# Performance work log

Measured on AMD Instinct MI355X. Metric: run time of the kernel, lower is better.

Reference implementation:

```python
import jax, jax.numpy as jnp
import numpy as np

N_NODES = 100000
N_EDGES = 1000000
VOCAB = 128
EMB = 64
HID = 64
N_CLASSES = 2
N_GRAPHS = 2048


def setup_inputs() -> dict:
    key = jax.random.key(0)
    ks = jax.random.split(key, 12)
    x = jax.random.randint(ks[0], (N_NODES,), 0, VOCAB)
    edge_index = jax.random.randint(ks[1], (2, N_EDGES), 0, N_NODES)
    batch = jnp.sort(jax.random.randint(ks[2], (N_NODES,), 0, N_GRAPHS))

    def glorot(k, shape):
        fan = shape[0]
        return jax.random.normal(k, shape, dtype=jnp.float32) / np.sqrt(fan).astype(np.float32)

    emb = jax.random.normal(ks[3], (VOCAB, EMB), dtype=jnp.float32)
    W1_l = glorot(ks[4], (EMB, HID)); b1 = jnp.zeros((HID,), jnp.float32)
    W1_r = glorot(ks[5], (EMB, HID))
    W2_l = glorot(ks[6], (HID, HID)); b2 = jnp.zeros((HID,), jnp.float32)
    W2_r = glorot(ks[7], (HID, HID))
    W_out = glorot(ks[8], (HID, N_CLASSES)); b_out = jnp.zeros((N_CLASSES,), jnp.float32)
    return {"x": x, "edge_index": edge_index, "batch": batch, "emb": emb,
            "W1_l": W1_l, "b1": b1, "W1_r": W1_r,
            "W2_l": W2_l, "b2": b2, "W2_r": W2_r,
            "W_out": W_out, "b_out": b_out}


def _sage_conv(h, src, dst, Wl, bl, Wr):
    # PyG SAGEConv: out = lin_l(mean_{j in N(i)} h_j) + lin_r(h_i); lin_r has no bias
    msgs = h[src]                                                        # [E, D] gather
    agg = jax.ops.segment_sum(msgs, dst, num_segments=N_NODES)          # [N, D] scatter-add
    cnt = jax.ops.segment_sum(jnp.ones((src.shape[0], 1), h.dtype), dst,
                              num_segments=N_NODES)                      # [N, 1] degree
    mean = agg / jnp.maximum(cnt, 1.0)
    return mean @ Wl + bl + h @ Wr


def reference(x, edge_index, batch, emb, W1_l, b1, W1_r, W2_l, b2, W2_r, W_out, b_out):
    src, dst = edge_index[0], edge_index[1]
    h = emb[x]                                                           # [N, EMB]
    h = jax.nn.relu(_sage_conv(h, src, dst, W1_l, b1, W1_r))             # [N, HID]
    h = jax.nn.relu(_sage_conv(h, src, dst, W2_l, b2, W2_r))             # [N, HID]
    # global_mean_pool over graph ids
    gsum = jax.ops.segment_sum(h, batch, num_segments=N_GRAPHS)          # [G, HID]
    gcnt = jax.ops.segment_sum(jnp.ones((N_NODES, 1), h.dtype), batch,
                               num_segments=N_GRAPHS)
    pooled = gsum / jnp.maximum(gcnt, 1.0)
    return pooled @ W_out + b_out                                        # [G, C]
```

## Files before the change

### kernel.cpp

```cpp
#include <hip/hip_runtime.h>
#include <hip/hip_bf16.h>

#define N_NODES 100000
#define N_EDGES 1000000
#define EMB 64
#define HID 64
#define VOCAB 128
#define N_GRAPHS 2048

#define CBUCKET 256
#define NBK ((N_NODES + CBUCKET - 1) / CBUCKET)
#define CAP 4096
#define CHUNK 4096
#define SCAT_BLOCKS ((N_EDGES + CHUNK - 1) / CHUNK)
#define GB ((N_NODES + 255) / 256)

#define BCASTF(v, l) __int_as_float(__builtin_amdgcn_readlane(__float_as_int(v), (l)))

typedef __attribute__((ext_vector_type(8))) short short8;
typedef __attribute__((ext_vector_type(4))) float f32x4;

__device__ __forceinline__ float bf2f(unsigned short u) {
    return __uint_as_float((unsigned)u << 16);
}
__device__ __forceinline__ unsigned short f2bf(float f) {
    return __bfloat16_as_ushort(__float2bfloat16(f));
}

__global__ __launch_bounds__(256) void setup_kernel(
    const int* __restrict__ batch, int* __restrict__ gstart,
    const float* __restrict__ emb, const float* __restrict__ W1l,
    const float* __restrict__ W1r,
    const float* __restrict__ W2l, const float* __restrict__ W2r,
    float* __restrict__ embW1l, float* __restrict__ embW1r,
    unsigned short* __restrict__ w2frag,
    int* __restrict__ cursor, float* __restrict__ gsum)
{
    int b = blockIdx.x;
    int t = threadIdx.x;
    if (b < GB) {
        int i = b * 256 + t;
        if (i >= N_NODES) return;
        int bg = batch[i];
        int bp = (i == 0) ? -1 : batch[i - 1];
        for (int g = bp + 1; g <= bg; ++g) gstart[g] = i;
        if (i == N_NODES - 1)
            for (int g = bg + 1; g <= N_GRAPHS; ++g) gstart[g] = N_NODES;
    } else if (b < GB + 32) {
        int vb = b - GB;
        int wave = t >> 6, lane = t & 63;
        int v = vb * 4 + wave;
        if (v < VOCAB) {
            float er = emb[v * 64 + lane];
            float al = 0.f, ar = 0.f;
#pragma unroll 8
            for (int d = 0; d < 64; ++d) {
                float e = BCASTF(er, d);
                al += e * W1l[d * 64 + lane];
                ar += e * W1r[d * 64 + lane];
            }
            embW1l[v * 64 + lane] = al;
            embW1r[v * 64 + lane] = ar;
        }
        int g = vb * 256 + t;
        int j = g & 7, l = (g >> 3) & 63, h = (g >> 9) & 1, tt = g >> 10;
        int k = h * 32 + ((l >> 4) * 8) + j;
        int n = tt * 16 + (l & 15);
        float w = (n < 64) ? W2l[k * 64 + n] : W2r[k * 64 + (n - 64)];
        w2frag[g] = f2bf(w);
    } else {
        for (int i = t; i < NBK; i += 256) cursor[i] = i * CAP;
        for (int i = t; i < N_GRAPHS * 2; i += 256) gsum[i] = 0.f;
    }
}

__global__ __launch_bounds__(256) void scatter_kernel(
    const int* __restrict__ src, const int* __restrict__ dst,
    const int* __restrict__ x,
    int* __restrict__ cursor, unsigned* __restrict__ edge8)
{
    __shared__ unsigned earr[CHUNK];
    __shared__ unsigned short karr[CHUNK];
    __shared__ int bcnt[NBK];
    __shared__ int bbase[NBK];
    int t = threadIdx.x;
    for (int i = t; i < NBK; i += 256) bcnt[i] = 0;
    __syncthreads();
    int e0 = blockIdx.x * CHUNK;
    int n = min(e0 + CHUNK, N_EDGES) - e0;
    for (int i = t; i < n; i += 256) {
        int d = dst[e0 + i];
        int s = src[e0 + i];
        int xv = x[s];
        int k = d >> 8;
        earr[i] = (unsigned)s | ((unsigned)xv << 17) | ((unsigned)(d & 255) << 24);
        karr[i] = (unsigned short)k;
        atomicAdd(&bcnt[k], 1);
    }
    __syncthreads();
    for (int i = t; i < NBK; i += 256) {
        int c = bcnt[i];
        bbase[i] = c ? atomicAdd(&cursor[i], c) : 0;
        bcnt[i] = 0;
    }
    __syncthreads();
    for (int i = t; i < n; i += 256) {
        int k = karr[i];
        int off = atomicAdd(&bcnt[k], 1);
        edge8[bbase[k] + off] = earr[i];
    }
}

__global__ __launch_bounds__(256) void csr_kernel(
    const unsigned* __restrict__ edge8, const int* __restrict__ cursor,
    int* __restrict__ row_start, int* __restrict__ deg, int* __restrict__ col)
{
    __shared__ int cnt[CBUCKET];
    __shared__ int scn[CBUCKET];
    int b = blockIdx.x;
    int t = threadIdx.x;
    int lo = b * CAP, hi = cursor[b];
    cnt[t] = 0;
    __syncthreads();
    for (int i = lo + t; i < hi; i += 256)
        atomicAdd(&cnt[edge8[i] >> 24], 1);
    __syncthreads();
    int v = cnt[t];
    scn[t] = v;
    __syncthreads();
    for (int off = 1; off < 256; off <<= 1) {
        int tmp = (t >= off) ? scn[t - off] : 0;
        __syncthreads();
        scn[t] += tmp;
        __syncthreads();
    }
    int excl = scn[t] - v;
    int node = b * CBUCKET + t;
    if (node < N_NODES) { row_start[node] = lo + excl; deg[node] = v; }
    cnt[t] = excl;
    __syncthreads();
    for (int i = lo + t; i < hi; i += 256) {
        unsigned e = edge8[i];
        int slot = atomicAdd(&cnt[e >> 24], 1);
        col[lo + slot] = (int)(e & 0xFFFFFF);
    }
}

#define S1_NPW 8
__global__ __launch_bounds__(256) void sage1_kernel(
    const int* __restrict__ x, const float* __restrict__ embW1l,
    const float* __restrict__ embW1r, const float* __restrict__ b1,
    const int* __restrict__ row_start, const int* __restrict__ deg,
    const int* __restrict__ col, unsigned short* __restrict__ h1b)
{
    __shared__ float elds[VOCAB * 64];
    int t = threadIdx.x;
    for (int i = t * 4; i < VOCAB * 64; i += 1024)
        *(float4*)&elds[i] = *(const float4*)&embW1l[i];
    __syncthreads();

    int wave = t >> 6, lane = t & 63;
    int base_node = (blockIdx.x * 4 + wave) * S1_NPW;
    float bias = b1[lane];

    int rs[S1_NPW], dgs[S1_NPW], cidx[S1_NPW], xn[S1_NPW];
    float self[S1_NPW];
#pragma unroll
    for (int n = 0; n < S1_NPW; ++n) {
        rs[n] = row_start[base_node + n];
        dgs[n] = deg[base_node + n];
        xn[n] = x[base_node + n];
    }
#pragma unroll
    for (int n = 0; n < S1_NPW; ++n) {
        cidx[n] = (lane < dgs[n]) ? col[rs[n] + lane] : 0;
        self[n] = embW1r[xn[n] * 64 + lane];
    }

    for (int n = 0; n < S1_NPW; ++n) {
        int node = base_node + n;
        int dg = dgs[n];
        int dgc = (dg < 64) ? dg : 64;

        float s0 = 0.f, s1 = 0.f, s2 = 0.f, s3 = 0.f;
        int j = 0;
        for (; j + 4 <= dgc; j += 4) {
            int x0 = __builtin_amdgcn_readlane(cidx[n], j + 0) >> 17;
            int x1 = __builtin_amdgcn_readlane(cidx[n], j + 1) >> 17;
            int x2 = __builtin_amdgcn_readlane(cidx[n], j + 2) >> 17;
            int x3 = __builtin_amdgcn_readlane(cidx[n], j + 3) >> 17;
            s0 += elds[x0 * 64 + lane];
            s1 += elds[x1 * 64 + lane];
            s2 += elds[x2 * 64 + lane];
            s3 += elds[x3 * 64 + lane];
        }
        for (; j < dgc; ++j) {
            int x0 = __builtin_amdgcn_readlane(cidx[n], j) >> 17;
            s0 += elds[x0 * 64 + lane];
        }
        for (int k = 64; k < dg; ++k) {
            int c = col[rs[n] + k];
            s0 += elds[(c >> 17) * 64 + lane];
        }
        float mean = ((s0 + s1) + (s2 + s3)) / fmaxf((float)dg, 1.0f);
        h1b[node * 64 + lane] = f2bf(fmaxf(mean + bias + self[n], 0.f));
    }
}

__global__ __launch_bounds__(256) void mfma_transform_kernel(
    const unsigned short* __restrict__ h1b,
    const unsigned short* __restrict__ w2frag,
    unsigned char* __restrict__ p8, unsigned short* __restrict__ q16)
{
    int wave = threadIdx.x >> 6, lane = threadIdx.x & 63;
    int base16 = blockIdx.x * 64 + wave * 16;
    if (base16 >= N_NODES) return;
    int m = lane & 15, quad = lane >> 4;

    const unsigned short* arow = h1b + (base16 + m) * 64 + quad * 8;
    short8 a0 = *(const short8*)(arow);
    short8 a1 = *(const short8*)(arow + 32);

#pragma unroll
    for (int tt = 0; tt < 8; ++tt) {
        short8 b0 = *(const short8*)(w2frag + (tt * 1024 + 0)   + lane * 8);
        short8 b1 = *(const short8*)(w2frag + (tt * 1024 + 512) + lane * 8);
        f32x4 acc = {0.f, 0.f, 0.f, 0.f};
        acc = __builtin_amdgcn_mfma_f32_16x16x32_bf16(a0, b0, acc, 0, 0, 0);
        acc = __builtin_amdgcn_mfma_f32_16x16x32_bf16(a1, b1, acc, 0, 0, 0);
        int o = tt * 16 + m;
        if (o < 64) {
            int pk01 = __builtin_amdgcn_cvt_pk_fp8_f32(acc[0], acc[1], 0, false);
            int pk23 = __builtin_amdgcn_cvt_pk_fp8_f32(acc[2], acc[3], 0, false);
            p8[(base16 + quad * 4 + 0) * 64 + o] = (unsigned char)(pk01 & 0xff);
            p8[(base16 + quad * 4 + 1) * 64 + o] = (unsigned char)((pk01 >> 8) & 0xff);
            p8[(base16 + quad * 4 + 2) * 64 + o] = (unsigned char)(pk23 & 0xff);
            p8[(base16 + quad * 4 + 3) * 64 + o] = (unsigned char)((pk23 >> 8) & 0xff);
        } else {
            int oc = o & 63;
#pragma unroll
            for (int i = 0; i < 4; ++i) {
                int node = base16 + quad * 4 + i;
                q16[node * 64 + oc] = f2bf(acc[i]);
            }
        }
    }
}

#define S2_NPW 8
__global__ __launch_bounds__(256, 8) void sage2_kernel(
    const unsigned char* __restrict__ p, const unsigned short* __restrict__ q,
    const int* __restrict__ row_start, const int* __restrict__ deg,
    const int* __restrict__ col, const float* __restrict__ b2,
    const float* __restrict__ Wout, const int* __restrict__ batch,
    float* __restrict__ gsum)
{
    int t = threadIdx.x;
    int wave = t >> 6, lane = t & 63;
    int base_node = (blockIdx.x * 4 + wave) * S2_NPW;
    int c = lane & 15;
    int g = lane >> 4;

    float4 b2v = ((const float4*)b2)[c];
    float4 w01 = ((const float4*)Wout)[c * 2];
    float4 w23 = ((const float4*)Wout)[c * 2 + 1];

    int rs[S2_NPW], dgs[S2_NPW], cidx[S2_NPW];
#pragma unroll
    for (int n = 0; n < S2_NPW; ++n) {
        rs[n] = row_start[base_node + n];
        dgs[n] = deg[base_node + n];
    }
#pragma unroll
    for (int n = 0; n < S2_NPW; ++n)
        cidx[n] = (lane < dgs[n]) ? (col[rs[n] + lane] & 0x1FFFF) : 0;

    for (int n = 0; n < S2_NPW; ++n) {
        int node = base_node + n;
        int dg = dgs[n];
        int dgc = (dg < 64) ? dg : 64;

        float4 a0 = {0.f,0.f,0.f,0.f}, a1 = {0.f,0.f,0.f,0.f};
        for (int j = 0; j < dgc; j += 8) {
            int jj0 = j + g, jj1 = j + 4 + g;
            int i0 = __shfl(cidx[n], jj0, 64);
            int i1 = __shfl(cidx[n], jj1, 64);
            unsigned v0 = *(const unsigned*)(p + i0 * 64 + c * 4);
            unsigned v1 = *(const unsigned*)(p + i1 * 64 + c * 4);
            if (jj0 < dgc) {
                a0.x += __builtin_amdgcn_cvt_f32_fp8(v0, 0);
                a0.y += __builtin_amdgcn_cvt_f32_fp8(v0, 1);
                a0.z += __builtin_amdgcn_cvt_f32_fp8(v0, 2);
                a0.w += __builtin_amdgcn_cvt_f32_fp8(v0, 3);
            }
            if (jj1 < dgc) {
                a1.x += __builtin_amdgcn_cvt_f32_fp8(v1, 0);
                a1.y += __builtin_amdgcn_cvt_f32_fp8(v1, 1);
                a1.z += __builtin_amdgcn_cvt_f32_fp8(v1, 2);
                a1.w += __builtin_amdgcn_cvt_f32_fp8(v1, 3);
            }
        }
        for (int k = 64; k < dg; ++k) {
            int r = col[rs[n] + k] & 0x1FFFF;
            unsigned v = *(const unsigned*)(p + r * 64 + c * 4);
            if (g == 0) {
                a0.x += __builtin_amdgcn_cvt_f32_fp8(v, 0);
                a0.y += __builtin_amdgcn_cvt_f32_fp8(v, 1);
                a0.z += __builtin_amdgcn_cvt_f32_fp8(v, 2);
                a0.w += __builtin_amdgcn_cvt_f32_fp8(v, 3);
            }
        }
        float sx = a0.x + a1.x, sy = a0.y + a1.y, sz = a0.z + a1.z, sw = a0.w + a1.w;
        sx += __shfl_xor(sx, 16, 64); sx += __shfl_xor(sx, 32, 64);
        sy += __shfl_xor(sy, 16, 64); sy += __shfl_xor(sy, 32, 64);
        sz += __shfl_xor(sz, 16, 64); sz += __shfl_xor(sz, 32, 64);
        sw += __shfl_xor(sw, 16, 64); sw += __shfl_xor(sw, 32, 64);

        float inv = 1.0f / fmaxf((float)dg, 1.0f);
        ushort4 qv = *(const ushort4*)(q + node * 64 + c * 4);
        float h0 = fmaxf(sx * inv + b2v.x + bf2f(qv.x), 0.f);
        float h1 = fmaxf(sy * inv + b2v.y + bf2f(qv.y), 0.f);
        float h2 = fmaxf(sz * inv + b2v.z + bf2f(qv.z), 0.f);
        float h3 = fmaxf(sw * inv + b2v.w + bf2f(qv.w), 0.f);

        float p0 = h0 * w01.x + h1 * w01.z + h2 * w23.x + h3 * w23.z;
        float p1 = h0 * w01.y + h1 * w01.w + h2 * w23.y + h3 * w23.w;
        if (g != 0) { p0 = 0.f; p1 = 0.f; }
        p0 += __shfl_down(p0, 8, 64);  p1 += __shfl_down(p1, 8, 64);
        p0 += __shfl_down(p0, 4, 64);  p1 += __shfl_down(p1, 4, 64);
        p0 += __shfl_down(p0, 2, 64);  p1 += __shfl_down(p1, 2, 64);
        p0 += __shfl_down(p0, 1, 64);  p1 += __shfl_down(p1, 1, 64);
        if (lane == 0) {
            int grp = batch[node];
            atomicAdd(&gsum[grp * 2 + 0], p0);
            atomicAdd(&gsum[grp * 2 + 1], p1);
        }
    }
}

__global__ __launch_bounds__(256) void finalize_kernel(
    const float* __restrict__ gsum, const int* __restrict__ gstart,
    const float* __restrict__ bout, float* __restrict__ out)
{
    int g = blockIdx.x * 256 + threadIdx.x;
    if (g >= N_GRAPHS) return;
    int cnt = gstart[g + 1] - gstart[g];
    float inv = 1.0f / fmaxf((float)cnt, 1.0f);
    out[g * 2 + 0] = gsum[g * 2 + 0] * inv + bout[0];
    out[g * 2 + 1] = gsum[g * 2 + 1] * inv + bout[1];
}

extern "C" void kernel_launch(void* const* d_in, const int* in_sizes, int n_in,
                              void* d_out, int out_size, void* d_ws, size_t ws_size,
                              hipStream_t stream) {
    const int*   x    = (const int*)  d_in[0];
    const int*   ei   = (const int*)  d_in[1];
    const int*   batch= (const int*)  d_in[2];
    const float* emb  = (const float*)d_in[3];
    const float* W1l  = (const float*)d_in[4];
    const float* b1   = (const float*)d_in[5];
    const float* W1r  = (const float*)d_in[6];
    const float* W2l  = (const float*)d_in[7];
    const float* b2   = (const float*)d_in[8];
    const float* W2r  = (const float*)d_in[9];
    const float* Wout = (const float*)d_in[10];
    const float* bout = (const float*)d_in[11];
    float* out = (float*)d_out;

    const int* src = ei;
    const int* dst = ei + N_EDGES;

    char* ws = (char*)d_ws;
    size_t off = 0;
    unsigned char*  p8     = (unsigned char*) (ws + off); off += (size_t)N_NODES * 64;
    unsigned short* q16    = (unsigned short*)(ws + off); off += (size_t)N_NODES * 64 * 2;
    unsigned short* h1b    = (unsigned short*)(ws + off); off += (size_t)N_NODES * 64 * 2;
    unsigned short* w2frag = (unsigned short*)(ws + off); off += (size_t)8192 * 2;
    float*    embW1l = (float*)   (ws + off); off += (size_t)VOCAB * 64 * 4;
    float*    embW1r = (float*)   (ws + off); off += (size_t)VOCAB * 64 * 4;
    int*      rowst  = (int*)     (ws + off); off += (size_t)N_NODES * 4;
    int*      deg    = (int*)     (ws + off); off += (size_t)N_NODES * 4;
    int*      col    = (int*)     (ws + off); off += (size_t)(NBK * CAP + 256) * 4;
    unsigned* edge8  = (unsigned*)(ws + off); off += (size_t)NBK * CAP * 4;
    int*      cursor = (int*)     (ws + off); off += (size_t)NBK * 4;
    int*      gstart = (int*)     (ws + off); off += (size_t)(N_GRAPHS + 1) * 4;
    float*    gsum   = (float*)   (ws + off); off += (size_t)N_GRAPHS * 2 * 4;

    setup_kernel<<<GB + 32 + 1, 256, 0, stream>>>(
        batch, gstart, emb, W1l, W1r, W2l, W2r, embW1l, embW1r, w2frag,
        cursor, gsum);
    scatter_kernel<<<SCAT_BLOCKS, 256, 0, stream>>>(src, dst, x, cursor, edge8);
    csr_kernel<<<NBK, 256, 0, stream>>>(edge8, cursor, rowst, deg, col);
    sage1_kernel<<<N_NODES / (4 * S1_NPW), 256, 0, stream>>>(
        x, embW1l, embW1r, b1, rowst, deg, col, h1b);
    mfma_transform_kernel<<<(N_NODES + 63) / 64, 256, 0, stream>>>(
        h1b, w2frag, p8, q16);
    sage2_kernel<<<N_NODES / (4 * S2_NPW), 256, 0, stream>>>(
        p8, q16, rowst, deg, col, b2, Wout, batch, gsum);
    finalize_kernel<<<(N_GRAPHS + 255) / 256, 256, 0, stream>>>(gsum, gstart, bout, out);
}
```

Baseline: 217.8 us.

## Fuse MFMA transform into sage1 and fold setup work into scatter kernel

The layer-2 MFMA projection now runs inside sage1. Each block stages its bf16 h1 rows in LDS, reusing the embedding table buffer, and runs the 16x16x32 MFMAs there, so the global h1b intermediate and its write and re-read disappear. The setup work (graph starts, emb·W1, w2frag packing) moves into extra blocks of the scatter kernel. Cursor and gsum initialisation becomes a hipMemsetAsync, with cursor offsets now relative to each bucket base. sage2's launch-bounds occupancy hint drops from 8 to 6, and the added LDS round trip and barriers in sage1 could lower its occupancy.

```diff
diff --git a/kernel.cpp b/kernel.cpp
--- a/kernel.cpp
+++ b/kernel.cpp
@@ -27,27 +27,60 @@
     return __bfloat16_as_ushort(__float2bfloat16(f));
 }
 
-__global__ __launch_bounds__(256) void setup_kernel(
+__global__ __launch_bounds__(256) void scatter_kernel(
+    const int* __restrict__ src, const int* __restrict__ dst,
+    const int* __restrict__ x,
+    int* __restrict__ cursor, unsigned* __restrict__ edge8,
     const int* __restrict__ batch, int* __restrict__ gstart,
     const float* __restrict__ emb, const float* __restrict__ W1l,
     const float* __restrict__ W1r,
     const float* __restrict__ W2l, const float* __restrict__ W2r,
     float* __restrict__ embW1l, float* __restrict__ embW1r,
-    unsigned short* __restrict__ w2frag,
-    int* __restrict__ cursor, float* __restrict__ gsum)
-{
+    unsigned short* __restrict__ w2frag)
+{
+    __shared__ unsigned earr[CHUNK];
+    __shared__ unsigned short karr[CHUNK];
+    __shared__ int bcnt[NBK];
+    __shared__ int bbase[NBK];
     int b = blockIdx.x;
     int t = threadIdx.x;
-    if (b < GB) {
-        int i = b * 256 + t;
+
+    if (b < SCAT_BLOCKS) {
+        for (int i = t; i < NBK; i += 256) bcnt[i] = 0;
+        __syncthreads();
+        int e0 = b * CHUNK;
+        int n = min(e0 + CHUNK, N_EDGES) - e0;
+        for (int i = t; i < n; i += 256) {
+            int d = dst[e0 + i];
+            int s = src[e0 + i];
+            int xv = x[s];
+            int k = d >> 8;
+            earr[i] = (unsigned)s | ((unsigned)xv << 17) | ((unsigned)(d & 255) << 24);
+            karr[i] = (unsigned short)k;
+            atomicAdd(&bcnt[k], 1);
+        }
+        __syncthreads();
+        for (int i = t; i < NBK; i += 256) {
+            int c = bcnt[i];
+            bbase[i] = i * CAP + (c ? atomicAdd(&cursor[i], c) : 0);
+            bcnt[i] = 0;
+        }
+        __syncthreads();
+        for (int i = t; i < n; i += 256) {
+            int k = karr[i];
+            int off = atomicAdd(&bcnt[k], 1);
+            edge8[bbase[k] + off] = earr[i];
+        }
+    } else if (b < SCAT_BLOCKS + GB) {
+        int i = (b - SCAT_BLOCKS) * 256 + t;
         if (i >= N_NODES) return;
         int bg = batch[i];
         int bp = (i == 0) ? -1 : batch[i - 1];
         for (int g = bp + 1; g <= bg; ++g) gstart[g] = i;
         if (i == N_NODES - 1)
             for (int g = bg + 1; g <= N_GRAPHS; ++g) gstart[g] = N_NODES;
-    } else if (b < GB + 32) {
-        int vb = b - GB;
+    } else {
+        int vb = b - SCAT_BLOCKS - GB;
         int wave = t >> 6, lane = t & 63;
         int v = vb * 4 + wave;
         if (v < VOCAB) {
@@ -68,46 +101,6 @@
         int n = tt * 16 + (l & 15);
         float w = (n < 64) ? W2l[k * 64 + n] : W2r[k * 64 + (n - 64)];
         w2frag[g] = f2bf(w);
-    } else {
-        for (int i = t; i < NBK; i += 256) cursor[i] = i * CAP;
-        for (int i = t; i < N_GRAPHS * 2; i += 256) gsum[i] = 0.f;
-    }
-}
-
-__global__ __launch_bounds__(256) void scatter_kernel(
-    const int* __restrict__ src, const int* __restrict__ dst,
-    const int* __restrict__ x,
-    int* __restrict__ cursor, unsigned* __restrict__ edge8)
-{
-    __shared__ unsigned earr[CHUNK];
-    __shared__ unsigned short karr[CHUNK];
-    __shared__ int bcnt[NBK];
-    __shared__ int bbase[NBK];
-    int t = threadIdx.x;
-    for (int i = t; i < NBK; i += 256) bcnt[i] = 0;
-    __syncthreads();
-    int e0 = blockIdx.x * CHUNK;
-    int n = min(e0 + CHUNK, N_EDGES) - e0;
-    for (int i = t; i < n; i += 256) {
-        int d = dst[e0 + i];
-        int s = src[e0 + i];
-        int xv = x[s];
-        int k = d >> 8;
-        earr[i] = (unsigned)s | ((unsigned)xv << 17) | ((unsigned)(d & 255) << 24);
-        karr[i] = (unsigned short)k;
-        atomicAdd(&bcnt[k], 1);
-    }
-    __syncthreads();
-    for (int i = t; i < NBK; i += 256) {
-        int c = bcnt[i];
-        bbase[i] = c ? atomicAdd(&cursor[i], c) : 0;
-        bcnt[i] = 0;
-    }
-    __syncthreads();
-    for (int i = t; i < n; i += 256) {
-        int k = karr[i];
-        int off = atomicAdd(&bcnt[k], 1);
-        edge8[bbase[k] + off] = earr[i];
     }
 }
 
@@ -119,7 +112,7 @@
     __shared__ int scn[CBUCKET];
     int b = blockIdx.x;
     int t = threadIdx.x;
-    int lo = b * CAP, hi = cursor[b];
+    int lo = b * CAP, hi = lo + cursor[b];
     cnt[t] = 0;
     __syncthreads();
     for (int i = lo + t; i < hi; i += 256)
@@ -151,7 +144,8 @@
     const int* __restrict__ x, const float* __restrict__ embW1l,
     const float* __restrict__ embW1r, const float* __restrict__ b1,
     const int* __restrict__ row_start, const int* __restrict__ deg,
-    const int* __restrict__ col, unsigned short* __restrict__ h1b)
+    const int* __restrict__ col, const unsigned short* __restrict__ w2frag,
+    unsigned char* __restrict__ p8, unsigned short* __restrict__ q16)
 {
     __shared__ float elds[VOCAB * 64];
     int t = threadIdx.x;
@@ -160,7 +154,8 @@
     __syncthreads();
 
     int wave = t >> 6, lane = t & 63;
-    int base_node = (blockIdx.x * 4 + wave) * S1_NPW;
+    int block_base = blockIdx.x * (4 * S1_NPW);
+    int base_node = block_base + wave * S1_NPW;
     float bias = b1[lane];
 
     int rs[S1_NPW], dgs[S1_NPW], cidx[S1_NPW], xn[S1_NPW];
@@ -177,8 +172,8 @@
         self[n] = embW1r[xn[n] * 64 + lane];
     }
 
+    float h1v[S1_NPW];
     for (int n = 0; n < S1_NPW; ++n) {
-        int node = base_node + n;
         int dg = dgs[n];
         int dgc = (dg < 64) ? dg : 64;
 
@@ -203,52 +198,49 @@
             s0 += elds[(c >> 17) * 64 + lane];
         }
         float mean = ((s0 + s1) + (s2 + s3)) / fmaxf((float)dg, 1.0f);
-        h1b[node * 64 + lane] = f2bf(fmaxf(mean + bias + self[n], 0.f));
-    }
-}
-
-__global__ __launch_bounds__(256) void mfma_transform_kernel(
-    const unsigned short* __restrict__ h1b,
-    const unsigned short* __restrict__ w2frag,
-    unsigned char* __restrict__ p8, unsigned short* __restrict__ q16)
-{
-    int wave = threadIdx.x >> 6, lane = threadIdx.x & 63;
-    int base16 = blockIdx.x * 64 + wave * 16;
-    if (base16 >= N_NODES) return;
+        h1v[n] = fmaxf(mean + bias + self[n], 0.f);
+    }
+    __syncthreads();
+
+    unsigned short* msbuf = (unsigned short*)elds;
+#pragma unroll
+    for (int n = 0; n < S1_NPW; ++n)
+        msbuf[(wave * S1_NPW + n) * 72 + lane] = f2bf(h1v[n]);
+    __syncthreads();
+
+    int grp = wave >> 1, tbase = (wave & 1) * 4;
     int m = lane & 15, quad = lane >> 4;
-
-    const unsigned short* arow = h1b + (base16 + m) * 64 + quad * 8;
+    int base16g = block_base + grp * 16;
+    const unsigned short* arow = &msbuf[(grp * 16 + m) * 72 + quad * 8];
     short8 a0 = *(const short8*)(arow);
     short8 a1 = *(const short8*)(arow + 32);
 
 #pragma unroll
-    for (int tt = 0; tt < 8; ++tt) {
-        short8 b0 = *(const short8*)(w2frag + (tt * 1024 + 0)   + lane * 8);
-        short8 b1 = *(const short8*)(w2frag + (tt * 1024 + 512) + lane * 8);
+    for (int tt = tbase; tt < tbase + 4; ++tt) {
+        short8 b0 = *(const short8*)(w2frag + tt * 1024 + lane * 8);
+        short8 b1v = *(const short8*)(w2frag + tt * 1024 + 512 + lane * 8);
         f32x4 acc = {0.f, 0.f, 0.f, 0.f};
         acc = __builtin_amdgcn_mfma_f32_16x16x32_bf16(a0, b0, acc, 0, 0, 0);
-        acc = __builtin_amdgcn_mfma_f32_16x16x32_bf16(a1, b1, acc, 0, 0, 0);
+        acc = __builtin_amdgcn_mfma_f32_16x16x32_bf16(a1, b1v, acc, 0, 0, 0);
         int o = tt * 16 + m;
         if (o < 64) {
             int pk01 = __builtin_amdgcn_cvt_pk_fp8_f32(acc[0], acc[1], 0, false);
             int pk23 = __builtin_amdgcn_cvt_pk_fp8_f32(acc[2], acc[3], 0, false);
-            p8[(base16 + quad * 4 + 0) * 64 + o] = (unsigned char)(pk01 & 0xff);
-            p8[(base16 + quad * 4 + 1) * 64 + o] = (unsigned char)((pk01 >> 8) & 0xff);
-            p8[(base16 + quad * 4 + 2) * 64 + o] = (unsigned char)(pk23 & 0xff);
-            p8[(base16 + quad * 4 + 3) * 64 + o] = (unsigned char)((pk23 >> 8) & 0xff);
+            p8[(base16g + quad * 4 + 0) * 64 + o] = (unsigned char)(pk01 & 0xff);
+            p8[(base16g + quad * 4 + 1) * 64 + o] = (unsigned char)((pk01 >> 8) & 0xff);
+            p8[(base16g + quad * 4 + 2) * 64 + o] = (unsigned char)(pk23 & 0xff);
+            p8[(base16g + quad * 4 + 3) * 64 + o] = (unsigned char)((pk23 >> 8) & 0xff);
         } else {
             int oc = o & 63;
 #pragma unroll
-            for (int i = 0; i < 4; ++i) {
-                int node = base16 + quad * 4 + i;
-                q16[node * 64 + oc] = f2bf(acc[i]);
-            }
+            for (int i = 0; i < 4; ++i)
+                q16[(base16g + quad * 4 + i) * 64 + oc] = f2bf(acc[i]);
         }
     }
 }
 
 #define S2_NPW 8
-__global__ __launch_bounds__(256, 8) void sage2_kernel(
+__global__ __launch_bounds__(256, 6) void sage2_kernel(
     const unsigned char* __restrict__ p, const unsigned short* __restrict__ q,
     const int* __restrict__ row_start, const int* __restrict__ deg,
     const int* __restrict__ col, const float* __restrict__ b2,
@@ -374,7 +366,6 @@
     size_t off = 0;
     unsigned char*  p8     = (unsigned char*) (ws + off); off += (size_t)N_NODES * 64;
     unsigned short* q16    = (unsigned short*)(ws + off); off += (size_t)N_NODES * 64 * 2;
-    unsigned short* h1b    = (unsigned short*)(ws + off); off += (size_t)N_NODES * 64 * 2;
     unsigned short* w2frag = (unsigned short*)(ws + off); off += (size_t)8192 * 2;
     float*    embW1l = (float*)   (ws + off); off += (size_t)VOCAB * 64 * 4;
     float*    embW1r = (float*)   (ws + off); off += (size_t)VOCAB * 64 * 4;
@@ -382,19 +373,18 @@
     int*      deg    = (int*)     (ws + off); off += (size_t)N_NODES * 4;
     int*      col    = (int*)     (ws + off); off += (size_t)(NBK * CAP + 256) * 4;
     unsigned* edge8  = (unsigned*)(ws + off); off += (size_t)NBK * CAP * 4;
+    int*      gstart = (int*)     (ws + off); off += (size_t)(N_GRAPHS + 1) * 4;
     int*      cursor = (int*)     (ws + off); off += (size_t)NBK * 4;
-    int*      gstart = (int*)     (ws + off); off += (size_t)(N_GRAPHS + 1) * 4;
     float*    gsum   = (float*)   (ws + off); off += (size_t)N_GRAPHS * 2 * 4;
 
-    setup_kernel<<<GB + 32 + 1, 256, 0, stream>>>(
-        batch, gstart, emb, W1l, W1r, W2l, W2r, embW1l, embW1r, w2frag,
-        cursor, gsum);
-    scatter_kernel<<<SCAT_BLOCKS, 256, 0, stream>>>(src, dst, x, cursor, edge8);
+    hipMemsetAsync(cursor, 0, (size_t)NBK * 4 + (size_t)N_GRAPHS * 2 * 4, stream);
+
+    scatter_kernel<<<SCAT_BLOCKS + GB + 32, 256, 0, stream>>>(
+        src, dst, x, cursor, edge8,
+        batch, gstart, emb, W1l, W1r, W2l, W2r, embW1l, embW1r, w2frag);
     csr_kernel<<<NBK, 256, 0, stream>>>(edge8, cursor, rowst, deg, col);
     sage1_kernel<<<N_NODES / (4 * S1_NPW), 256, 0, stream>>>(
-        x, embW1l, embW1r, b1, rowst, deg, col, h1b);
-    mfma_transform_kernel<<<(N_NODES + 63) / 64, 256, 0, stream>>>(
-        h1b, w2frag, p8, q16);
+        x, embW1l, embW1r, b1, rowst, deg, col, w2frag, p8, q16);
     sage2_kernel<<<N_NODES / (4 * S2_NPW), 256, 0, stream>>>(
         p8, q16, rowst, deg, col, b2, Wout, batch, gsum);
     finalize_kernel<<<(N_GRAPHS + 255) / 256, 256, 0, stream>>>(gsum, gstart, bout, out);
```

Measured after the change: 210.5 us. -3.3%, faster.
